# Kernel tuning notes

Hardware: AMD Instinct MI355X
Metric: run time of the kernel (lower is better)

The kernel has to match this reference:

```python
import jax, jax.numpy as jnp
import numpy as np

WINDOW_SIZE = 11
SIGMA = 1.5
C1 = 0.01 ** 2
C2 = 0.03 ** 2


def _gaussian_window(window_size, channel, dtype):
    coords = jnp.arange(window_size, dtype=jnp.float32) - window_size // 2
    g = jnp.exp(-(coords ** 2) / (2.0 * SIGMA ** 2))
    g = g / g.sum()
    w2d = jnp.outer(g, g)  # [K, K]
    # depthwise kernel: [channel, 1, K, K] (OIHW with feature_group_count=channel)
    return jnp.broadcast_to(w2d, (channel, 1, window_size, window_size)).astype(dtype)


def _dwconv(x, window, channel):
    pad = WINDOW_SIZE // 2
    return jax.lax.conv_general_dilated(
        x, window,
        window_strides=(1, 1),
        padding=[(pad, pad), (pad, pad)],
        dimension_numbers=('NCHW', 'OIHW', 'NCHW'),
        feature_group_count=channel,
    )


def _ssim(img1, img2):
    channel = img1.shape[1]
    window = _gaussian_window(WINDOW_SIZE, channel, img1.dtype)
    mu1 = _dwconv(img1, window, channel)
    mu2 = _dwconv(img2, window, channel)
    mu1_sq = mu1 * mu1
    mu2_sq = mu2 * mu2
    mu1_mu2 = mu1 * mu2
    sigma1_sq = _dwconv(img1 * img1, window, channel) - mu1_sq
    sigma2_sq = _dwconv(img2 * img2, window, channel) - mu2_sq
    sigma12 = _dwconv(img1 * img2, window, channel) - mu1_mu2
    ssim_map = ((2.0 * mu1_mu2 + C1) * (2.0 * sigma12 + C2)) / (
        (mu1_sq + mu2_sq + C1) * (sigma1_sq + sigma2_sq + C2))
    return ssim_map.mean()


def setup_inputs() -> dict:
    key = jax.random.key(0)
    k1, k2 = jax.random.split(key)
    img1 = jax.random.uniform(k1, (32, 3, 512, 512), dtype=jnp.float32)
    img2 = jax.random.uniform(k2, (32, 3, 512, 512), dtype=jnp.float32)
    return {"img1": img1, "img2": img2}


def reference(img1, img2):
    return _ssim(img1, img2)
```

## Files before the change

### kernel.cpp

```cpp
#include <hip/hip_runtime.h>
#include <cmath>

#define IMG_H 512
#define IMG_W 512
#define TH 32
#define TW 64
#define LDSW 83
#define NPLANES 96
#define NPIX 25165824.0

typedef float vf2 __attribute__((ext_vector_type(2)));

struct GaussW { float w[11]; };

__global__ __launch_bounds__(256, 3) void ssim_main(
    const float* __restrict__ img1, const float* __restrict__ img2,
    float* __restrict__ partials, GaussW gw, int use_atomic, float* __restrict__ out)
{
    __shared__ vf2   VAB[TH][LDSW];
    __shared__ vf2   VPQ[TH][LDSW];
    __shared__ float VS [TH][LDSW];
    __shared__ float wsum[4];

    const int tid = threadIdx.x;
    const int plane = blockIdx.z;
    const int tr0 = blockIdx.y * TH;
    const int tc0 = blockIdx.x * TW;
    const float* __restrict__ plane1 = img1 + ((size_t)plane << 18);
    const float* __restrict__ plane2 = img2 + ((size_t)plane << 18);

    {
        const int j = tid % 80;
        const int chunk = tid / 80;
        if (chunk < 3) {
            const int r0 = chunk * 11;
            const int gc = tc0 + j - 8;
            const float cmask = (gc >= 0 && gc < IMG_W) ? 1.f : 0.f;
            const int gcc = min(max(gc, 0), IMG_W - 1);

            vf2 aAB[11], aPQ[11];
            float aS[11];

            #pragma unroll
            for (int ii = 0; ii < 21; ++ii) {
                const int gr = tr0 + r0 - 5 + ii;
                const float rmask = (gr >= 0 && gr < IMG_H) ? cmask : 0.f;
                const int grc = min(max(gr, 0), IMG_H - 1);
                const uint32_t idx = (uint32_t)(grc * IMG_W + gcc);
                const float a = plane1[idx] * rmask;
                const float b = plane2[idx] * rmask;
                const vf2 ab = { a, b };
                const vf2 pq = ab * ab;
                const float s = a * b;
                #pragma unroll
                for (int o = 0; o < 11; ++o) {
                    if (o <= ii && ii <= o + 10) {
                        const float wt = gw.w[ii - o];
                        const vf2 wtv = { wt, wt };
                        if (ii == o) {
                            aAB[o] = wtv * ab;
                            aPQ[o] = wtv * pq;
                            aS[o]  = wt * s;
                        } else {
                            aAB[o] = __builtin_elementwise_fma(wtv, ab, aAB[o]);
                            aPQ[o] = __builtin_elementwise_fma(wtv, pq, aPQ[o]);
                            aS[o]  = fmaf(wt, s, aS[o]);
                        }
                    }
                }
            }
            #pragma unroll
            for (int o = 0; o < 11; ++o) {
                const int r = r0 + o;
                if (r0 + o < TH) {
                    VAB[r][j] = aAB[o];
                    VPQ[r][j] = aPQ[o];
                    VS [r][j] = aS[o];
                }
            }
        }
    }
    __syncthreads();

    float lsum = 0.f;
    {
        const int r = tid & 31;
        const int c0 = (tid >> 5) * 8;
        const vf2*   __restrict__ bAB = &VAB[r][c0];
        const vf2*   __restrict__ bPQ = &VPQ[r][c0];
        const float* __restrict__ bS  = &VS [r][c0];

        vf2 mAB[8], ePQ[8];
        float e12[8];

        #pragma unroll
        for (int k = 3; k <= 20; ++k) {
            const vf2   vab = bAB[k];
            const vf2   vpq = bPQ[k];
            const float vs  = bS[k];
            #pragma unroll
            for (int c = 0; c < 8; ++c) {
                if (k - 13 <= c && c <= k - 3) {
                    const float wt = gw.w[k - 3 - c];
                    const vf2 wtv = { wt, wt };
                    if (k == c + 3) {
                        mAB[c] = wtv * vab;
                        ePQ[c] = wtv * vpq;
                        e12[c] = wt * vs;
                    } else {
                        mAB[c] = __builtin_elementwise_fma(wtv, vab, mAB[c]);
                        ePQ[c] = __builtin_elementwise_fma(wtv, vpq, ePQ[c]);
                        e12[c] = fmaf(wt, vs, e12[c]);
                    }
                }
            }
        }
        #pragma unroll
        for (int c = 0; c < 8; ++c) {
            const float a1 = mAB[c].x, a2 = mAB[c].y;
            const float den1 = fmaf(a1, a1, fmaf(a2, a2, 0.0001f));
            const float s11  = fmaf(-a1, a1, ePQ[c].x);
            const float s22  = fmaf(-a2, a2, ePQ[c].y);
            const float s12  = fmaf(-a1, a2, e12[c]);
            const float mu12 = a1 * a2;
            const float num  = fmaf(2.f, mu12, 0.0001f) * fmaf(2.f, s12, 0.0009f);
            const float den  = den1 * (s11 + s22 + 0.0009f);
            lsum = fmaf(num, __builtin_amdgcn_rcpf(den), lsum);
        }
    }
    #pragma unroll
    for (int off = 32; off; off >>= 1) lsum += __shfl_down(lsum, off, 64);
    if ((tid & 63) == 0) wsum[tid >> 6] = lsum;
    __syncthreads();
    if (tid == 0) {
        const float bs = wsum[0] + wsum[1] + wsum[2] + wsum[3];
        if (use_atomic) {
            atomicAdd(out, bs * (float)(1.0 / NPIX));
        } else {
            const int bId = (blockIdx.z * gridDim.y + blockIdx.y) * gridDim.x + blockIdx.x;
            partials[bId] = bs;
        }
    }
}

__global__ __launch_bounds__(256) void ssim_reduce(
    const float* __restrict__ partials, int n, float* __restrict__ out)
{
    const int tid = threadIdx.x;
    double s = 0.0;
    for (int i = tid; i < n; i += 256) s += (double)partials[i];
    #pragma unroll
    for (int off = 32; off; off >>= 1) s += __shfl_down(s, off, 64);
    __shared__ double ws[4];
    if ((tid & 63) == 0) ws[tid >> 6] = s;
    __syncthreads();
    if (tid == 0) out[0] = (float)(((ws[0] + ws[1]) + (ws[2] + ws[3])) / NPIX);
}

extern "C" void kernel_launch(void* const* d_in, const int* in_sizes, int n_in,
                              void* d_out, int out_size, void* d_ws, size_t ws_size,
                              hipStream_t stream) {
    const float* img1 = (const float*)d_in[0];
    const float* img2 = (const float*)d_in[1];
    float* out = (float*)d_out;

    GaussW gw;
    {
        double g[11], sum = 0.0;
        for (int i = 0; i < 11; ++i) {
            const double c = (double)(i - 5);
            g[i] = std::exp(-(c * c) / 4.5);
            sum += g[i];
        }
        for (int i = 0; i < 11; ++i) gw.w[i] = (float)(g[i] / sum);
    }

    dim3 grid(IMG_W / TW, IMG_H / TH, NPLANES);
    const int nPart = grid.x * grid.y * grid.z;

    if (ws_size >= (size_t)nPart * sizeof(float)) {
        ssim_main<<<grid, 256, 0, stream>>>(img1, img2, (float*)d_ws, gw, 0, out);
        ssim_reduce<<<1, 256, 0, stream>>>((float*)d_ws, nPart, out);
    } else {
        hipMemsetAsync(d_out, 0, sizeof(float), stream);
        ssim_main<<<grid, 256, 0, stream>>>(img1, img2, nullptr, gw, 1, out);
    }
}
```

Baseline: 109.2 us.

## Vectorize vertical pass over column pairs and restructure LDS into planar row layout

The vertical Gaussian pass now has each thread handle two adjacent columns with float2 global loads, and computes 8 output rows from 18 input rows instead of 11 from 21, using 160 threads instead of 240. The LDS storage changes from three interleaved arrays to one planar row buffer holding five 80-wide planes, with a row stride chosen to limit bank conflicts. Gaussian weights are pre-broadcast into vf2 registers and pinned with an empty asm so packed FMAs can use them. The aim is fewer load instructions and better packed-math use, at the cost of more registers per thread and more vertical-pass rows re-read per output row.

Result: slower. 119.9 us (+9.8%).

```diff
diff --git a/kernel.cpp b/kernel.cpp
--- a/kernel.cpp
+++ b/kernel.cpp
@@ -5,7 +5,9 @@
 #define IMG_W 512
 #define TH 32
 #define TW 64
-#define LDSW 83
+#define NCOL 80
+#define PL 80
+#define ROWSTRIDE 402
 #define NPLANES 96
 #define NPIX 25165824.0
 
@@ -17,9 +19,7 @@
     const float* __restrict__ img1, const float* __restrict__ img2,
     float* __restrict__ partials, GaussW gw, int use_atomic, float* __restrict__ out)
 {
-    __shared__ vf2   VAB[TH][LDSW];
-    __shared__ vf2   VPQ[TH][LDSW];
-    __shared__ float VS [TH][LDSW];
+    __shared__ float L[TH * ROWSTRIDE];
     __shared__ float wsum[4];
 
     const int tid = threadIdx.x;
@@ -29,54 +29,61 @@
     const float* __restrict__ plane1 = img1 + ((size_t)plane << 18);
     const float* __restrict__ plane2 = img2 + ((size_t)plane << 18);
 
+    vf2 wv[11];
+    #pragma unroll
+    for (int t = 0; t < 11; ++t) { wv[t].x = gw.w[t]; wv[t].y = gw.w[t]; }
+    #pragma unroll
+    for (int t = 0; t < 11; ++t) asm("" : "+v"(wv[t]));
+
     {
-        const int j = tid % 80;
-        const int chunk = tid / 80;
-        if (chunk < 3) {
-            const int r0 = chunk * 11;
-            const int gc = tc0 + j - 8;
-            const float cmask = (gc >= 0 && gc < IMG_W) ? 1.f : 0.f;
-            const int gcc = min(max(gc, 0), IMG_W - 1);
+        const int p = tid % 40;
+        const int chunk = tid / 40;
+        if (chunk < 4) {
+            const int r0 = chunk * 8;
+            const int gc = tc0 + 2 * p - 8;
+            const bool cok = (unsigned)gc < IMG_W;
+            const int gcc = min(max(gc, 0), IMG_W - 2);
 
-            vf2 aAB[11], aPQ[11];
-            float aS[11];
+            vf2 aA[8], aB[8], aP[8], aQ[8], aS[8];
 
             #pragma unroll
-            for (int ii = 0; ii < 21; ++ii) {
+            for (int ii = 0; ii < 18; ++ii) {
                 const int gr = tr0 + r0 - 5 + ii;
-                const float rmask = (gr >= 0 && gr < IMG_H) ? cmask : 0.f;
+                const float m = ((unsigned)gr < IMG_H) & cok ? 1.f : 0.f;
                 const int grc = min(max(gr, 0), IMG_H - 1);
-                const uint32_t idx = (uint32_t)(grc * IMG_W + gcc);
-                const float a = plane1[idx] * rmask;
-                const float b = plane2[idx] * rmask;
-                const vf2 ab = { a, b };
-                const vf2 pq = ab * ab;
-                const float s = a * b;
+                const uint32_t off = (uint32_t)(grc * IMG_W + gcc);
+                vf2 a2 = *(const vf2*)(plane1 + off);
+                vf2 b2 = *(const vf2*)(plane2 + off);
+                a2.x *= m; a2.y *= m; b2.x *= m; b2.y *= m;
+                const vf2 p2 = a2 * a2;
+                const vf2 q2 = b2 * b2;
+                const vf2 s2 = a2 * b2;
                 #pragma unroll
-                for (int o = 0; o < 11; ++o) {
+                for (int o = 0; o < 8; ++o) {
                     if (o <= ii && ii <= o + 10) {
-                        const float wt = gw.w[ii - o];
-                        const vf2 wtv = { wt, wt };
+                        const vf2 w2 = wv[ii - o];
                         if (ii == o) {
-                            aAB[o] = wtv * ab;
-                            aPQ[o] = wtv * pq;
-                            aS[o]  = wt * s;
+                            aA[o] = w2 * a2; aB[o] = w2 * b2; aP[o] = w2 * p2;
+                            aQ[o] = w2 * q2; aS[o] = w2 * s2;
                         } else {
-                            aAB[o] = __builtin_elementwise_fma(wtv, ab, aAB[o]);
-                            aPQ[o] = __builtin_elementwise_fma(wtv, pq, aPQ[o]);
-                            aS[o]  = fmaf(wt, s, aS[o]);
+                            aA[o] = __builtin_elementwise_fma(w2, a2, aA[o]);
+                            aB[o] = __builtin_elementwise_fma(w2, b2, aB[o]);
+                            aP[o] = __builtin_elementwise_fma(w2, p2, aP[o]);
+                            aQ[o] = __builtin_elementwise_fma(w2, q2, aQ[o]);
+                            aS[o] = __builtin_elementwise_fma(w2, s2, aS[o]);
                         }
                     }
                 }
             }
+            const int j = 2 * p;
             #pragma unroll
-            for (int o = 0; o < 11; ++o) {
-                const int r = r0 + o;
-                if (r0 + o < TH) {
-                    VAB[r][j] = aAB[o];
-                    VPQ[r][j] = aPQ[o];
-                    VS [r][j] = aS[o];
-                }
+            for (int o = 0; o < 8; ++o) {
+                float* row = &L[(r0 + o) * ROWSTRIDE];
+                *(vf2*)&row[j]          = aA[o];
+                *(vf2*)&row[PL + j]     = aB[o];
+                *(vf2*)&row[2 * PL + j] = aP[o];
+                *(vf2*)&row[3 * PL + j] = aQ[o];
+                *(vf2*)&row[4 * PL + j] = aS[o];
             }
         }
     }
@@ -86,30 +93,30 @@
     {
         const int r = tid & 31;
         const int c0 = (tid >> 5) * 8;
-        const vf2*   __restrict__ bAB = &VAB[r][c0];
-        const vf2*   __restrict__ bPQ = &VPQ[r][c0];
-        const float* __restrict__ bS  = &VS [r][c0];
+        const float* row  = &L[r * ROWSTRIDE + c0];
+        const float* row2 = row + 2 * PL;
 
         vf2 mAB[8], ePQ[8];
         float e12[8];
 
         #pragma unroll
         for (int k = 3; k <= 20; ++k) {
-            const vf2   vab = bAB[k];
-            const vf2   vpq = bPQ[k];
-            const float vs  = bS[k];
+            vf2 vab, vpq;
+            vab.x = row[k];  vab.y = row[PL + k];
+            vpq.x = row2[k]; vpq.y = row2[PL + k];
+            const float vs = row2[2 * PL + k];
             #pragma unroll
             for (int c = 0; c < 8; ++c) {
                 if (k - 13 <= c && c <= k - 3) {
+                    const vf2 w2 = wv[k - 3 - c];
                     const float wt = gw.w[k - 3 - c];
-                    const vf2 wtv = { wt, wt };
                     if (k == c + 3) {
-                        mAB[c] = wtv * vab;
-                        ePQ[c] = wtv * vpq;
+                        mAB[c] = w2 * vab;
+                        ePQ[c] = w2 * vpq;
                         e12[c] = wt * vs;
                     } else {
-                        mAB[c] = __builtin_elementwise_fma(wtv, vab, mAB[c]);
-                        ePQ[c] = __builtin_elementwise_fma(wtv, vpq, ePQ[c]);
+                        mAB[c] = __builtin_elementwise_fma(w2, vab, mAB[c]);
+                        ePQ[c] = __builtin_elementwise_fma(w2, vpq, ePQ[c]);
                         e12[c] = fmaf(wt, vs, e12[c]);
                     }
                 }
```
